# Kernel optimization log

Measured on AMD Instinct MI355X. Metric: run time of the kernel, lower is better.

## Reference

```python
import jax, jax.numpy as jnp
import numpy as np
from jax import lax

F8 = jnp.float8_e4m3fn


def setup_inputs() -> dict:
    key = jax.random.key(0)
    kx, kw = jax.random.split(key)
    x = jax.random.normal(kx, (2, 128, 4, 192, 320), dtype=jnp.float32)
    # matches reset_parameters: normal(0, 0.02) then cast to fp8
    weight = jax.random.normal(kw, (128, 128, 3, 3, 3), dtype=jnp.float32) * 0.02
    return {"x": x, "weight": weight}


def reference(x, weight):
    # fp8 e4m3 quantization round-trip (the torch module stores/consumes fp8),
    # compute/accumulate in fp32 as an fp8 conv kernel would.
    xq = x.astype(F8).astype(jnp.float32)
    wq = weight.astype(F8).astype(jnp.float32)
    # causal temporal padding: (kT-1, 0) = (2, 0); spatial 'same' padding (1,1)
    xp = jnp.pad(xq, ((0, 0), (0, 0), (2, 0), (1, 1), (1, 1)))
    out = lax.conv_general_dilated(
        xp, wq,
        window_strides=(1, 1, 1),
        padding='VALID',
        dimension_numbers=('NCDHW', 'OIDHW', 'NCDHW'),
    )  # (B, 128, 4, 192, 320)
    return out
```

## Files before the change

kernel.cpp:

```cpp
#include <hip/hip_runtime.h>
#include <hip/hip_fp8.h>


using f32x16 = __attribute__((ext_vector_type(16))) float;
using i32x8 = __attribute__((ext_vector_type(8))) int;
using i32x4 = __attribute__((ext_vector_type(4))) int;
typedef long long i64;
struct alignas(16) L2v { i64 x, y; };

namespace {
constexpr int Cc = 128, Dd = 4, Hh = 192, Ww = 320;
constexpr int HP = 194, WP = 322;
constexpr int NTAP = 27;
constexpr size_t PLANE = (size_t)4 * WP * 32;
constexpr size_t XQ_BYTES = (size_t)2 * Dd * HP * PLANE;
constexpr int ZA = 8 * 2 * 2576;
constexpr int ZB = 8 * 192 * 32;
constexpr int GSTR = WP * 32;
constexpr int HB = 1056;
constexpr int KDSTR = 9 * 2 * 4 * 64 * 32;
constexpr int NQX = 5 * 192 * 8;
constexpr int NZP = (ZA + ZB + 255) / 256;
constexpr int NWP = (Cc * Cc * NTAP + 255) / 256;
}

__global__ __launch_bounds__(256) void prep_kernel(const float* __restrict__ x,
                                                   const float* __restrict__ w,
                                                   unsigned char* __restrict__ xq,
                                                   unsigned char* __restrict__ wpk) {
  const int id = blockIdx.x;
  const int tid = threadIdx.x;
  if (id < NQX) {
    __shared__ unsigned char lt[64 * 136];
    const int wx = id % 5;
    const int h = (id / 5) % 192;
    const int bd = id / 960;
    const int b = bd >> 2, d = bd & 3;
    const int w0 = wx * 64;
    const int wl = tid & 63, cig = tid >> 6;
    const size_t cstr = (size_t)Dd * Hh * Ww;
    const float* xp = x + (((size_t)b * Cc * Dd + d) * Hh + h) * Ww + w0 + wl;
    #pragma unroll 4
    for (int i = 0; i < 32; ++i) {
      int ci = cig * 32 + i;
      __hip_fp8_e4m3 q(xp[ci * cstr]);
      lt[wl * 136 + ci] = q.__x;
    }
    __syncthreads();
    unsigned char* plane = xq + ((size_t)(b * Dd + d) * HP + h + 1) * PLANE;
    int g = tid >> 6, ww = tid & 63;
    const unsigned char* src = lt + ww * 136 + g * 32;
    i64 a0 = *(const i64*)(src), a1 = *(const i64*)(src + 8);
    i64 a2 = *(const i64*)(src + 16), a3 = *(const i64*)(src + 24);
    unsigned char* dst = plane + (size_t)g * GSTR + (size_t)(w0 + 1 + ww) * 32;
    *(L2v*)dst = L2v{a0, a1};
    *(L2v*)(dst + 16) = L2v{a2, a3};
  } else if (id < NQX + NZP) {
    int i = (id - NQX) * 256 + tid;
    if (i < ZA) {
      int bd = i / (2 * 2576);
      int r = i - bd * (2 * 2576);
      int hsel = r / 2576, seg = r - hsel * 2576;
      L2v z{0, 0};
      *(L2v*)(xq + ((size_t)bd * HP + (hsel ? 193 : 0)) * PLANE + (size_t)seg * 16) = z;
    } else if (i < ZA + ZB) {
      int j = i - ZA;
      int bd = j / (192 * 32);
      int r = j - bd * (192 * 32);
      int h = r / 32 + 1;
      int t = r & 31;
      int g = t >> 3, s2 = t & 7;
      int wsel = s2 >> 2, part = s2 & 3;
      *(i64*)(xq + ((size_t)bd * HP + h) * PLANE + (size_t)g * GSTR
              + (size_t)(wsel ? 321 : 0) * 32 + part * 8) = 0;
    }
  } else {
    int idx = (id - NQX - NZP) * 256 + tid;
    if (idx < Cc * Cc * NTAP) {
      int tap = idx % NTAP;
      int t = idx / NTAP;
      int ci = t % Cc, co = t / Cc;
      int cc = ci >> 6, cq = co >> 5;
      int lane = (((ci >> 5) & 1) << 5) | (co & 31);
      __hip_fp8_e4m3 q(w[idx]);
      wpk[((((size_t)tap * 2 + cc) * 4 + cq) * 64 + lane) * 32 + (ci & 31)] = q.__x;
    }
  }
}

__global__ __launch_bounds__(256, 2) void conv_mfma(const unsigned char* __restrict__ xq,
                                                    const unsigned char* __restrict__ wpk,
                                                    float* __restrict__ out) {
  __shared__ unsigned char lb[6 * 4 * 2 * HB];
  const int tid = threadIdx.x;
  const int lane = tid & 63;
  const int hr = tid >> 6;
  const int l31 = lane & 31, chalf = lane >> 5;
  const int id = blockIdx.x;
  const int xcd = id & 7, j = id >> 3;
  const int h0l = j / 40, rem = j - h0l * 40;
  const int z = rem / 5, wx = rem - z * 5;
  const int b = z >> 2, dout = z & 3;
  const int h0 = (xcd * 6 + h0l) * 4;
  const int w0 = wx * 64;
  const int kdmin = dout >= 2 ? 0 : 2 - dout;

  const long imgstep = (long)HP * PLANE;
  const long img0 = (long)(b * Dd + dout - 2) * imgstep;
  const unsigned char* vbase = wpk + lane * 32;

  const unsigned char* bb[3];
  #pragma unroll
  for (int kw = 0; kw < 3; ++kw)
    bb[kw] = lb + hr * 8448 + chalf * 2112 + (l31 + kw) * 16;

  f32x16 acc[4][2];
  #pragma unroll
  for (int a = 0; a < 4; ++a)
    #pragma unroll
    for (int n = 0; n < 2; ++n)
      #pragma unroll
      for (int r = 0; r < 16; ++r) acc[a][n][r] = 0.f;

  for (int kd = kdmin; kd < 3; ++kd) {
    __syncthreads();
    const unsigned char* img = xq + img0 + (long)kd * imgstep;
    for (int u = tid; u < 1584; u += 256) {
      int w = u % 66, rest = u / 66;
      int g = rest & 3, hrow = rest >> 2;
      const unsigned char* src = img + (size_t)(h0 + hrow) * PLANE
          + (size_t)g * GSTR + (size_t)(w0 + w) * 32;
      L2v lo = *(const L2v*)src;
      L2v hi = *(const L2v*)(src + 16);
      unsigned char* base = lb + rest * 2112 + w * 16;
      *(L2v*)(base) = lo;
      *(L2v*)(base + HB) = hi;
    }
    __syncthreads();

    const unsigned char* wkd = vbase + (size_t)kd * KDSTR;
    __builtin_amdgcn_s_setprio(1);
    #pragma unroll
    for (int kh = 0; kh < 3; ++kh)
      #pragma unroll
      for (int cc = 0; cc < 2; ++cc)
        #pragma unroll
        for (int kw = 0; kw < 3; ++kw) {
          i32x8 av[4];
          #pragma unroll
          for (int ct = 0; ct < 4; ++ct)
            av[ct] = *(const i32x8*)(wkd + (kh * 3 + kw) * 16384 + cc * 8192 + ct * 2048);
          i32x8 bv[2];
          #pragma unroll
          for (int nf = 0; nf < 2; ++nf) {
            const int off = kh * 8448 + cc * 4224 + nf * 512;
            i32x4 blo = *(const i32x4*)(bb[kw] + off);
            i32x4 bhi = *(const i32x4*)(bb[kw] + off + HB);
            bv[nf] = __builtin_shufflevector(blo, bhi, 0, 1, 2, 3, 4, 5, 6, 7);
          }
          #pragma unroll
          for (int nf = 0; nf < 2; ++nf)
            #pragma unroll
            for (int ct = 0; ct < 4; ++ct)
              acc[ct][nf] = __builtin_amdgcn_mfma_scale_f32_32x32x64_f8f6f4(
                  av[ct], bv[nf], acc[ct][nf], 0, 0, 0, 127, 0, 127);
        }
    __builtin_amdgcn_s_setprio(0);
  }

  #pragma unroll
  for (int ct = 0; ct < 4; ++ct)
    #pragma unroll
    for (int nf = 0; nf < 2; ++nf) {
      int ww = w0 + nf * 32 + l31;
      #pragma unroll
      for (int reg = 0; reg < 16; ++reg) {
        int co = ct * 32 + (reg & 3) + 8 * (reg >> 2) + 4 * chalf;
        out[(((size_t)b * Cc + co) * Dd + dout) * (size_t)(Hh * Ww)
            + (size_t)(h0 + hr) * Ww + ww] = acc[ct][nf][reg];
      }
    }
}

extern "C" void kernel_launch(void* const* d_in, const int* in_sizes, int n_in,
                              void* d_out, int out_size, void* d_ws, size_t ws_size,
                              hipStream_t stream) {
  const float* x = (const float*)d_in[0];
  const float* w = (const float*)d_in[1];
  unsigned char* xq = (unsigned char*)d_ws;
  unsigned char* wpk = xq + XQ_BYTES;
  float* out = (float*)d_out;

  prep_kernel<<<dim3(NQX + NZP + NWP), 256, 0, stream>>>(x, w, xq, wpk);
  conv_mfma<<<dim3(1920), 256, 0, stream>>>(xq, wpk, out);
}
```

Before: 237.2 us.

## Halve rows per block, split output channels across waves, use global_load_lds

Each block now covers 2 output rows instead of 4, and the four waves are split into 2 rows by 2 output-channel halves. This doubles the grid to 3840 blocks, halves accumulator registers, and raises the occupancy hint to 4 blocks per CU. The input tile is staged with direct global-to-LDS loads instead of register round trips. The price is a larger relative halo (4 staged rows for 2 output rows), so more input is reloaded across blocks, and each wave now reads weights for only half the channels.

```diff
diff --git a/kernel.cpp b/kernel.cpp
--- a/kernel.cpp
+++ b/kernel.cpp
@@ -17,7 +17,7 @@
 constexpr int ZA = 8 * 2 * 2576;
 constexpr int ZB = 8 * 192 * 32;
 constexpr int GSTR = WP * 32;
-constexpr int HB = 1056;
+constexpr int REG = 16896;
 constexpr int KDSTR = 9 * 2 * 4 * 64 * 32;
 constexpr int NQX = 5 * 192 * 8;
 constexpr int NZP = (ZA + ZB + 255) / 256;
@@ -88,35 +88,61 @@
   }
 }
 
-__global__ __launch_bounds__(256, 2) void conv_mfma(const unsigned char* __restrict__ xq,
+__device__ __forceinline__ void gll16(const unsigned char* g, unsigned char* l) {
+  __builtin_amdgcn_global_load_lds(
+      (const __attribute__((address_space(1))) void*)g,
+      (__attribute__((address_space(3))) void*)l, 16, 0, 0);
+}
+
+__global__ __launch_bounds__(256, 4) void conv_mfma(const unsigned char* __restrict__ xq,
                                                     const unsigned char* __restrict__ wpk,
                                                     float* __restrict__ out) {
-  __shared__ unsigned char lb[6 * 4 * 2 * HB];
+  __shared__ unsigned char lb[2 * REG];
   const int tid = threadIdx.x;
-  const int lane = tid & 63;
-  const int hr = tid >> 6;
+  const int lane = tid & 63, wv = tid >> 6;
   const int l31 = lane & 31, chalf = lane >> 5;
+  const int hr = wv >> 1, ch = wv & 1;
   const int id = blockIdx.x;
   const int xcd = id & 7, j = id >> 3;
   const int h0l = j / 40, rem = j - h0l * 40;
   const int z = rem / 5, wx = rem - z * 5;
   const int b = z >> 2, dout = z & 3;
-  const int h0 = (xcd * 6 + h0l) * 4;
+  const int h0 = (xcd * 12 + h0l) * 2;
   const int w0 = wx * 64;
   const int kdmin = dout >= 2 ? 0 : 2 - dout;
 
   const long imgstep = (long)HP * PLANE;
   const long img0 = (long)(b * Dd + dout - 2) * imgstep;
-  const unsigned char* vbase = wpk + lane * 32;
+  const unsigned char* vbase = wpk + ch * 4096 + lane * 32;
+
+  size_t soff[4];
+  int ldst[4];
+  #pragma unroll
+  for (int k = 0; k < 4; ++k) {
+    int u = tid + k * 256;
+    int w = u % 66, rest = u / 66;
+    int g = rest & 3, hrow = rest >> 2;
+    soff[k] = (size_t)(h0 + hrow) * PLANE + (size_t)g * GSTR + (size_t)(w0 + w) * 32;
+    ldst[k] = u * 16;
+  }
+  size_t soff4;
+  int ldst4;
+  {
+    int u = 1024 + (tid & 31);
+    int w = u % 66, rest = u / 66;
+    int g = rest & 3, hrow = rest >> 2;
+    soff4 = (size_t)(h0 + hrow) * PLANE + (size_t)g * GSTR + (size_t)(w0 + w) * 32;
+    ldst4 = u * 16;
+  }
 
   const unsigned char* bb[3];
   #pragma unroll
   for (int kw = 0; kw < 3; ++kw)
-    bb[kw] = lb + hr * 8448 + chalf * 2112 + (l31 + kw) * 16;
-
-  f32x16 acc[4][2];
-  #pragma unroll
-  for (int a = 0; a < 4; ++a)
+    bb[kw] = lb + (hr * 4 + chalf) * 1056 + (l31 + kw) * 16;
+
+  f32x16 acc[2][2];
+  #pragma unroll
+  for (int a = 0; a < 2; ++a)
     #pragma unroll
     for (int n = 0; n < 2; ++n)
       #pragma unroll
@@ -125,16 +151,14 @@
   for (int kd = kdmin; kd < 3; ++kd) {
     __syncthreads();
     const unsigned char* img = xq + img0 + (long)kd * imgstep;
-    for (int u = tid; u < 1584; u += 256) {
-      int w = u % 66, rest = u / 66;
-      int g = rest & 3, hrow = rest >> 2;
-      const unsigned char* src = img + (size_t)(h0 + hrow) * PLANE
-          + (size_t)g * GSTR + (size_t)(w0 + w) * 32;
-      L2v lo = *(const L2v*)src;
-      L2v hi = *(const L2v*)(src + 16);
-      unsigned char* base = lb + rest * 2112 + w * 16;
-      *(L2v*)(base) = lo;
-      *(L2v*)(base + HB) = hi;
+    #pragma unroll
+    for (int k = 0; k < 4; ++k) {
+      gll16(img + soff[k], lb + ldst[k]);
+      gll16(img + soff[k] + 16, lb + REG + ldst[k]);
+    }
+    if (tid < 32) {
+      gll16(img + soff4, lb + ldst4);
+      gll16(img + soff4 + 16, lb + REG + ldst4);
     }
     __syncthreads();
 
@@ -146,36 +170,33 @@
       for (int cc = 0; cc < 2; ++cc)
         #pragma unroll
         for (int kw = 0; kw < 3; ++kw) {
-          i32x8 av[4];
+          i32x8 av[2];
           #pragma unroll
-          for (int ct = 0; ct < 4; ++ct)
+          for (int ct = 0; ct < 2; ++ct)
             av[ct] = *(const i32x8*)(wkd + (kh * 3 + kw) * 16384 + cc * 8192 + ct * 2048);
-          i32x8 bv[2];
           #pragma unroll
           for (int nf = 0; nf < 2; ++nf) {
-            const int off = kh * 8448 + cc * 4224 + nf * 512;
+            const int off = kh * 4224 + cc * 2112 + nf * 512;
             i32x4 blo = *(const i32x4*)(bb[kw] + off);
-            i32x4 bhi = *(const i32x4*)(bb[kw] + off + HB);
-            bv[nf] = __builtin_shufflevector(blo, bhi, 0, 1, 2, 3, 4, 5, 6, 7);
+            i32x4 bhi = *(const i32x4*)(bb[kw] + off + REG);
+            i32x8 bv = __builtin_shufflevector(blo, bhi, 0, 1, 2, 3, 4, 5, 6, 7);
+            #pragma unroll
+            for (int ct = 0; ct < 2; ++ct)
+              acc[ct][nf] = __builtin_amdgcn_mfma_scale_f32_32x32x64_f8f6f4(
+                  av[ct], bv, acc[ct][nf], 0, 0, 0, 127, 0, 127);
           }
-          #pragma unroll
-          for (int nf = 0; nf < 2; ++nf)
-            #pragma unroll
-            for (int ct = 0; ct < 4; ++ct)
-              acc[ct][nf] = __builtin_amdgcn_mfma_scale_f32_32x32x64_f8f6f4(
-                  av[ct], bv[nf], acc[ct][nf], 0, 0, 0, 127, 0, 127);
         }
     __builtin_amdgcn_s_setprio(0);
   }
 
   #pragma unroll
-  for (int ct = 0; ct < 4; ++ct)
+  for (int ct = 0; ct < 2; ++ct)
     #pragma unroll
     for (int nf = 0; nf < 2; ++nf) {
       int ww = w0 + nf * 32 + l31;
       #pragma unroll
       for (int reg = 0; reg < 16; ++reg) {
-        int co = ct * 32 + (reg & 3) + 8 * (reg >> 2) + 4 * chalf;
+        int co = ch * 64 + ct * 32 + (reg & 3) + 8 * (reg >> 2) + 4 * chalf;
         out[(((size_t)b * Cc + co) * Dd + dout) * (size_t)(Hh * Ww)
             + (size_t)(h0 + hr) * Ww + ww] = acc[ct][nf][reg];
       }
@@ -192,5 +213,5 @@
   float* out = (float*)d_out;
 
   prep_kernel<<<dim3(NQX + NZP + NWP), 256, 0, stream>>>(x, w, xq, wpk);
-  conv_mfma<<<dim3(1920), 256, 0, stream>>>(xq, wpk, out);
-}
+  conv_mfma<<<dim3(3840), 256, 0, stream>>>(xq, wpk, out);
+}
```

New measurement: 223.7 us. -5.7%, faster.
